# Kernel optimization log

Measured on AMD Instinct MI355X. Metric: run time of the kernel, lower is better.

The kernel has to match this reference:

```python
import jax, jax.numpy as jnp
import numpy as np

IMG = 32            # feature-map side == image_size
B, HC = 8, 3        # batch, hint channels
C, NH, L = 256, 8, 8  # model_channels, nhead, num_encoder_layers
DFF = 1025
HIN = IMG * 8       # hint resolution (three stride-2 convs => /8)
NEIGH = (7, 7)
CONV_SHAPES = [(16, HC), (16, 16), (32, 16), (32, 32), (96, 32), (96, 96), (256, 96), (C, 256)]
STRIDES = [1, 1, 2, 1, 2, 1, 2, 1]


def setup_inputs() -> dict:
    key = jax.random.key(0)
    ks = jax.random.split(key, 32)
    inp = {"hint": jax.random.normal(ks[0], (B, HC, HIN, HIN), jnp.float32)}
    for i, (co, ci) in enumerate(CONV_SHAPES):
        inp[f"conv_w{i}"] = jax.random.normal(ks[1 + i], (co, ci, 3, 3), jnp.float32) * 0.05
    base = 9
    def p(shape, j):
        return jax.random.normal(ks[base + j], (L,) + shape, jnp.float32) * 0.02
    inp["in_proj_w"] = p((3 * C, C), 0)
    inp["in_proj_b"] = p((3 * C,), 1)
    inp["out_w"] = p((C, C), 2)
    inp["out_b"] = p((C,), 3)
    inp["lin1_w"] = p((DFF, C), 4)
    inp["lin1_b"] = p((DFF,), 5)
    inp["lin2_w"] = p((C, DFF), 6)
    inp["lin2_b"] = p((C,), 7)
    inp["ln1_w"] = jnp.ones((L, C), jnp.float32)
    inp["ln1_b"] = jnp.zeros((L, C), jnp.float32)
    inp["ln2_w"] = jnp.ones((L, C), jnp.float32)
    inp["ln2_b"] = jnp.zeros((L, C), jnp.float32)
    return inp


def _conv(x, w, s):
    # torch Conv2d(k=3, padding=1, stride=s, bias=False)
    return jax.lax.conv_general_dilated(x, w, (s, s), [(1, 1), (1, 1)],
                                        dimension_numbers=("NCHW", "OIHW", "NCHW"))


def _sine_pos(h, w, c):
    # DETR/UniAD PositionEmbeddingSine (normalize=False, temperature=1e4) -> (h*w, c)
    npf = c // 2
    y = jnp.broadcast_to(jnp.arange(1, h + 1, dtype=jnp.float32)[:, None], (h, w))
    x = jnp.broadcast_to(jnp.arange(1, w + 1, dtype=jnp.float32)[None, :], (h, w))
    dim_t = 10000.0 ** (2.0 * (jnp.arange(npf, dtype=jnp.float32) // 2) / npf)
    px = x[..., None] / dim_t
    py = y[..., None] / dim_t
    px = jnp.stack([jnp.sin(px[..., 0::2]), jnp.cos(px[..., 1::2])], -1).reshape(h, w, npf)
    py = jnp.stack([jnp.sin(py[..., 0::2]), jnp.cos(py[..., 1::2])], -1).reshape(h, w, npf)
    return jnp.concatenate([py, px], -1).reshape(h * w, c)


def _neigh_mask(h, w, hm, wm):
    # vectorized version of generate_mask: 0 inside the hm x wm neighborhood, -inf outside
    ih = jnp.arange(h)
    iw = jnp.arange(w)
    dh = jnp.abs(ih[:, None] - ih[None, :]) <= hm // 2   # (h, h)
    dw = jnp.abs(iw[:, None] - iw[None, :]) <= wm // 2   # (w, w)
    allowed = (dh[:, None, :, None] & dw[None, :, None, :]).reshape(h * w, h * w)
    return jnp.where(allowed, 0.0, -1e9).astype(jnp.float32)


def _ln(x, g, b):
    mu = x.mean(-1, keepdims=True)
    v = ((x - mu) ** 2).mean(-1, keepdims=True)
    return (x - mu) / jnp.sqrt(v + 1e-5) * g + b


def _forward(hint, conv_ws, params):
    x = hint
    for i, (w, s) in enumerate(zip(conv_ws, STRIDES)):
        x = _conv(x, w, s)
        if i < len(conv_ws) - 1:
            x = jax.nn.silu(x)
    b, c, h, w = x.shape
    src = x.reshape(b, c, h * w).transpose(0, 2, 1)          # (B, N, C), N h-major
    pos = _sine_pos(h, w, c)[None]                           # (1, N, C)
    mask = _neigh_mask(h, w, *NEIGH)                         # (N, N)
    dh = c // NH
    scale = 1.0 / np.sqrt(dh).astype(np.float32)

    def layer(s, p):
        ipw, ipb, ow, ob, l1w, l1b, l2w, l2b, g1, b1, g2, b2 = p
        qk_in = s + pos
        q = (qk_in @ ipw[:c].T + ipb[:c]).reshape(b, -1, NH, dh)
        k = (qk_in @ ipw[c:2 * c].T + ipb[c:2 * c]).reshape(b, -1, NH, dh)
        v = (s @ ipw[2 * c:].T + ipb[2 * c:]).reshape(b, -1, NH, dh)
        sc = jnp.einsum('bnhd,bmhd->bhnm', q, k) * scale + mask
        a = jax.nn.softmax(sc, -1)
        ctx = jnp.einsum('bhnm,bmhd->bnhd', a, v).reshape(b, -1, c)
        s = _ln(s + ctx @ ow.T + ob, g1, b1)                 # post-norm
        ff = jax.nn.relu(s @ l1w.T + l1b) @ l2w.T + l2b      # dropout inactive (eval)
        return _ln(s + ff, g2, b2), None

    src, _ = jax.lax.scan(layer, src, params)
    return src.transpose(0, 2, 1).reshape(b, c, h, w)        # '(h w) b c -> b c h w'


def reference(hint, conv_w0, conv_w1, conv_w2, conv_w3, conv_w4, conv_w5, conv_w6, conv_w7,
              in_proj_w, in_proj_b, out_w, out_b, lin1_w, lin1_b, lin2_w, lin2_b,
              ln1_w, ln1_b, ln2_w, ln2_b):
    conv_ws = (conv_w0, conv_w1, conv_w2, conv_w3, conv_w4, conv_w5, conv_w6, conv_w7)
    params = (in_proj_w, in_proj_b, out_w, out_b, lin1_w, lin1_b, lin2_w, lin2_b,
              ln1_w, ln1_b, ln2_w, ln2_b)
    return _forward(hint, conv_ws, params)
```

## Files before the change

kernel.cpp:

```cpp
#include <hip/hip_runtime.h>
#include <hip/hip_bf16.h>


typedef __bf16 bf16x8 __attribute__((ext_vector_type(8)));
typedef float f32x4 __attribute__((ext_vector_type(4)));
typedef unsigned short us8v __attribute__((ext_vector_type(8)));

__device__ __forceinline__ unsigned short f2bf(float f) {
  unsigned int u = __float_as_uint(f);
  unsigned int r = (u + 0x7fffu + ((u >> 16) & 1u)) >> 16;
  return (unsigned short)r;
}
__device__ __forceinline__ float bf2f(unsigned short h) {
  return __uint_as_float(((unsigned int)h) << 16);
}

#define GLD16(src, dst)                                                        \
  __builtin_amdgcn_global_load_lds(                                            \
      (const __attribute__((address_space(1))) unsigned int*)(src),            \
      (__attribute__((address_space(3))) unsigned int*)(dst), 16, 0, 0)

template<int BM, int BN, int NT, int MODE, int LNF = 0, int KTC = 0>
__global__ __launch_bounds__(NT) void k_gemm(
    const unsigned short* __restrict__ A, int lda,
    const unsigned short* __restrict__ Bw, int ldb,
    const float* __restrict__ bias, const float* __restrict__ posadd,
    float* __restrict__ C, unsigned short* __restrict__ Cb, int ldc,
    int K, int Nstore, int act, int omode, long long zsB, long long zsC,
    const unsigned short* __restrict__ zpage, int Ci, int Hi, int stride, int lw,
    int divm, int divs, const float* __restrict__ lng, const float* __restrict__ lnb)
{
  constexpr int NW = NT / 64;
  constexpr int NWN = (NT == 512) ? 4 : ((BN >= 128) ? 2 : 1);
  constexpr int NWM = NW / NWN;
  constexpr int WM = BM / NWM, WN = BN / NWN;
  constexpr int MF = WM / 16, NF = WN / 16;
  constexpr int AIS = (BM * 8) / NT;
  constexpr int BIS = (BN * 8) / NT;
  __shared__ unsigned short lA[2][BM * 64];
  __shared__ unsigned short lB[2][BN * 64];
  int tid = threadIdx.x, lane = tid & 63, wid = tid >> 6;
  int bm = blockIdx.x * BM, bn = blockIdx.y * BN;
  const unsigned short* Bz = Bw + (size_t)blockIdx.z * zsB;

  int j = (lane & 7) ^ (lane >> 3);
  int e8 = (j & 3) << 3;
  int halfl = j >> 2;

  size_t arow[AIS], brow[BIS];
  int hb[AIS], wb[AIS];
  size_t ab[AIS];
#pragma unroll
  for (int i = 0; i < AIS; ++i) {
    int rr = (wid + i * NW) * 8 + (lane >> 3);
    if constexpr (MODE == 0) {
      arow[i] = (size_t)(bm + rr) * lda + (j << 3);
    } else {
      int pos = bm + rr;
      int b = pos >> (2 * lw);
      int rem = pos & ((1 << (2 * lw)) - 1);
      int ho = rem >> lw, wo = rem & ((1 << lw) - 1);
      hb[i] = ho * stride - 1;
      wb[i] = wo * stride - 1;
      ab[i] = (size_t)b * Hi * Hi * Ci;
    }
  }
#pragma unroll
  for (int i = 0; i < BIS; ++i)
    brow[i] = (size_t)(bn + (wid + i * NW) * 8 + (lane >> 3)) * ldb + (j << 3);

  auto stage = [&](int buf, int kt) {
    if constexpr (MODE == 1) {
      int s0 = kt * 2, s1 = s0 + 1;
      int t0 = (s0 * divm) >> divs, t1 = (s1 * divm) >> divs;
      int cipw = Ci >> 5;
      int cc0 = (s0 - t0 * cipw) << 5, cc1 = (s1 - t1 * cipw) << 5;
      int kh0 = (t0 * 171) >> 9, kw0 = t0 - kh0 * 3;
      int kh1 = (t1 * 171) >> 9, kw1 = t1 - kh1 * 3;
      int kh = halfl ? kh1 : kh0;
      int kw = halfl ? kw1 : kw0;
      int cco = halfl ? cc1 : cc0;
      bool tv = (halfl ? t1 : t0) < 9;
#pragma unroll
      for (int i = 0; i < AIS; ++i) {
        int hi = hb[i] + kh, wi = wb[i] + kw;
        const unsigned short* ap =
            (tv && (unsigned)hi < (unsigned)Hi && (unsigned)wi < (unsigned)Hi)
                ? (A + ab[i] + (size_t)(hi * Hi + wi) * Ci + cco + e8)
                : zpage;
        GLD16(ap, &lA[buf][(wid + i * NW) * 512]);
      }
    } else {
#pragma unroll
      for (int i = 0; i < AIS; ++i)
        GLD16(A + arow[i] + kt * 64, &lA[buf][(wid + i * NW) * 512]);
    }
#pragma unroll
    for (int i = 0; i < BIS; ++i)
      GLD16(Bz + brow[i] + kt * 64, &lB[buf][(wid + i * NW) * 512]);
  };

  f32x4 acc[MF][NF];
#pragma unroll
  for (int m = 0; m < MF; ++m)
#pragma unroll
    for (int n = 0; n < NF; ++n)
#pragma unroll
      for (int q = 0; q < 4; ++q) acc[m][n][q] = 0.f;

  int wn = wid % NWN, wm = wid / NWN;
  int r0 = wm * WM + (lane & 15);
  int c0 = wn * WN + (lane & 15);
  int sl0 = (((lane >> 4)) ^ (lane & 7)) << 3;
  int sl1 = (((lane >> 4) + 4) ^ (lane & 7)) << 3;
  const int nkt = (KTC > 0) ? KTC : (K >> 6);
  int cur = 0;
  stage(0, 0);
#pragma unroll
  for (int kt = 0; kt < nkt; ++kt) {
    if (kt + 1 < nkt) {
      stage(cur ^ 1, kt + 1);
      asm volatile("s_waitcnt vmcnt(%0)" : : "n"(AIS + BIS) : "memory");
    } else {
      asm volatile("s_waitcnt vmcnt(0)" : : : "memory");
    }
    __builtin_amdgcn_s_barrier();
    asm volatile("" ::: "memory");
    bf16x8 a0[MF], a1[MF], b0[NF], b1[NF];
#pragma unroll
    for (int m = 0; m < MF; ++m) {
      a0[m] = *(const bf16x8*)&lA[cur][(r0 + m * 16) * 64 + sl0];
      a1[m] = *(const bf16x8*)&lA[cur][(r0 + m * 16) * 64 + sl1];
    }
#pragma unroll
    for (int n = 0; n < NF; ++n) {
      b0[n] = *(const bf16x8*)&lB[cur][(c0 + n * 16) * 64 + sl0];
      b1[n] = *(const bf16x8*)&lB[cur][(c0 + n * 16) * 64 + sl1];
    }
#pragma unroll
    for (int m = 0; m < MF; ++m)
#pragma unroll
      for (int n = 0; n < NF; ++n)
        acc[m][n] = __builtin_amdgcn_mfma_f32_16x16x32_bf16(a0[m], b0[n], acc[m][n], 0, 0, 0);
#pragma unroll
    for (int m = 0; m < MF; ++m)
#pragma unroll
      for (int n = 0; n < NF; ++n)
        acc[m][n] = __builtin_amdgcn_mfma_f32_16x16x32_bf16(a1[m], b1[n], acc[m][n], 0, 0, 0);
    asm volatile("" ::: "memory");
    __builtin_amdgcn_s_barrier();
    cur ^= 1;
  }

  int colb = bn + wn * WN + (lane & 15);
  int rowb = bm + wm * WM + ((lane >> 4) << 2);
  float* Cz = C ? C + (size_t)blockIdx.z * zsC : nullptr;
  unsigned short* Cbz = Cb ? Cb + (size_t)blockIdx.z * zsC : nullptr;
#pragma unroll
  for (int n = 0; n < NF; ++n) {
    int col = colb + n * 16;
    if (col >= Nstore) continue;
    float bs = bias ? bias[col] : 0.f;
#pragma unroll
    for (int m = 0; m < MF; ++m) {
#pragma unroll
      for (int q = 0; q < 4; ++q) {
        int row = rowb + m * 16 + q;
        float v = acc[m][n][q] + bs;
        if (posadd && col < 512) v += posadd[((row & 1023) << 9) + col];
        if (act == 1) v = fmaxf(v, 0.f);
        else if (act == 2) v = v / (1.f + __expf(-v));
        size_t off = (size_t)row * ldc + col;
        if (omode == 0) Cz[off] = v;
        else if (omode == 1) Cbz[off] = f2bf(v);
        else { Cz[off] = v; Cbz[off] = f2bf(v); }
      }
    }
  }
}

__global__ __launch_bounds__(256) void k_mlp(
    const unsigned short* __restrict__ ctx, const unsigned short* __restrict__ wo,
    const float* __restrict__ ob,
    const unsigned short* __restrict__ w1, const float* __restrict__ b1,
    const unsigned short* __restrict__ w2, const float* __restrict__ b2,
    float* __restrict__ src, unsigned short* __restrict__ sbo,
    const float* __restrict__ g1, const float* __restrict__ lb1,
    const float* __restrict__ g2, const float* __restrict__ lb2)
{
  __shared__ unsigned short aT[4][32 * 64];
  __shared__ unsigned short lB[4][128 * 64];
  __shared__ unsigned short ffl[32][1160];
  __shared__ float red[2][32][2];
  int tid = threadIdx.x, lane = tid & 63, wid = tid >> 6;
  int bm = blockIdx.x << 5;
  int rsrc = lane >> 3;
  int jj8 = ((lane & 7) ^ rsrc) << 3;

  {
    int rr = wid * 8 + rsrc;
    const unsigned short* ap = ctx + (size_t)(bm + rr) * 256 + jj8;
#pragma unroll
    for (int kt = 0; kt < 4; ++kt)
      GLD16(ap + kt * 64, &aT[kt][wid * 512]);
  }

  auto issue = [&](int s) {
    const unsigned short* base;
    int ld, coloff, row0;
    if (s < 8)       { base = wo; ld = 256;  coloff = (s >> 1) * 64; row0 = (s & 1) * 128; }
    else if (s < 44) { int t = s - 8;  base = w1; ld = 256;  coloff = (t & 3) * 64; row0 = (t >> 2) * 128; }
    else             { int t = s - 44; base = w2; ld = 1152; coloff = (t >> 1) * 64; row0 = (t & 1) * 128; }
    int buf = s & 3;
#pragma unroll
    for (int i = 0; i < 4; ++i) {
      int rr = row0 + (wid + i * 4) * 8 + rsrc;
      GLD16(base + (size_t)rr * ld + coloff + jj8, &lB[buf][(wid + i * 4) * 512]);
    }
  };
  issue(0); issue(1); issue(2); issue(3);

  int wn = wid & 1, wm = wid >> 1;
  int r0 = wm * 16 + (lane & 15);
  int sl0 = ((lane >> 4) ^ (lane & 7)) << 3;
  int sl1 = (((lane >> 4) + 4) ^ (lane & 7)) << 3;
  int kqa = (lane >> 4) << 3;
  int cbase = wn * 16 + (lane & 15);
  int rowl = wm * 16 + ((lane >> 4) << 2);

  f32x4 acco[8];
#pragma unroll
  for (int m = 0; m < 8; ++m)
#pragma unroll
    for (int q = 0; q < 4; ++q) acco[m][q] = 0.f;
#pragma unroll
  for (int s = 0; s < 8; ++s) {
    const int kt = s >> 1, rh = s & 1;
    asm volatile("s_waitcnt vmcnt(12)" ::: "memory");
    __builtin_amdgcn_s_barrier();
    asm volatile("" ::: "memory");
    bf16x8 a0 = *(const bf16x8*)&aT[kt][r0 * 64 + sl0];
    bf16x8 a1 = *(const bf16x8*)&aT[kt][r0 * 64 + sl1];
    bf16x8 b0v[4], b1v[4];
#pragma unroll
    for (int nn = 0; nn < 4; ++nn) {
      int rowb = cbase + nn * 32;
      b0v[nn] = *(const bf16x8*)&lB[s & 3][rowb * 64 + sl0];
      b1v[nn] = *(const bf16x8*)&lB[s & 3][rowb * 64 + sl1];
    }
    __builtin_amdgcn_s_setprio(1);
#pragma unroll
    for (int nn = 0; nn < 4; ++nn)
      acco[rh * 4 + nn] = __builtin_amdgcn_mfma_f32_16x16x32_bf16(a0, b0v[nn], acco[rh * 4 + nn], 0, 0, 0);
#pragma unroll
    for (int nn = 0; nn < 4; ++nn)
      acco[rh * 4 + nn] = __builtin_amdgcn_mfma_f32_16x16x32_bf16(a1, b1v[nn], acco[rh * 4 + nn], 0, 0, 0);
    __builtin_amdgcn_s_setprio(0);
    asm volatile("" ::: "memory");
    __builtin_amdgcn_s_barrier();
    issue(s + 4);
  }

  float resid[8][4];
  {
    float x[8][4];
    float sums[4] = {0.f, 0.f, 0.f, 0.f}, sqs[4] = {0.f, 0.f, 0.f, 0.f};
#pragma unroll
    for (int m = 0; m < 8; ++m) {
      int col = ((m >> 2) << 7) + cbase + ((m & 3) << 5);
      float bs = ob[col];
#pragma unroll
      for (int q = 0; q < 4; ++q) {
        float v = acco[m][q] + bs + src[(size_t)(bm + rowl + q) * 256 + col];
        x[m][q] = v;
        sums[q] += v;
        sqs[q] += v * v;
      }
    }
#pragma unroll
    for (int q = 0; q < 4; ++q) {
      sums[q] += __shfl_xor(sums[q], 1); sqs[q] += __shfl_xor(sqs[q], 1);
      sums[q] += __shfl_xor(sums[q], 2); sqs[q] += __shfl_xor(sqs[q], 2);
      sums[q] += __shfl_xor(sums[q], 4); sqs[q] += __shfl_xor(sqs[q], 4);
      sums[q] += __shfl_xor(sums[q], 8); sqs[q] += __shfl_xor(sqs[q], 8);
    }
    if ((lane & 15) == 0) {
#pragma unroll
      for (int q = 0; q < 4; ++q) {
        red[wn][rowl + q][0] = sums[q];
        red[wn][rowl + q][1] = sqs[q];
      }
    }
    asm volatile("s_waitcnt lgkmcnt(0)" ::: "memory");
    __builtin_amdgcn_s_barrier();
    asm volatile("" ::: "memory");
#pragma unroll
    for (int q = 0; q < 4; ++q) {
      float ts = sums[q] + red[wn ^ 1][rowl + q][0];
      float tq = sqs[q] + red[wn ^ 1][rowl + q][1];
      float mu = ts * (1.f / 256.f);
      float var = tq * (1.f / 256.f) - mu * mu;
      float rs = rsqrtf(var + 1e-5f);
      int r = rowl + q;
#pragma unroll
      for (int m = 0; m < 8; ++m) {
        int col = ((m >> 2) << 7) + cbase + ((m & 3) << 5);
        float o = (x[m][q] - mu) * rs * g1[col] + lb1[col];
        resid[m][q] = o;
        int kt = col >> 6, jjc = (col >> 3) & 7, e = col & 7;
        aT[kt][r * 64 + ((jjc ^ (r & 7)) << 3) + e] = f2bf(o);
      }
    }
  }
  asm volatile("s_waitcnt lgkmcnt(0)" ::: "memory");
  __builtin_amdgcn_s_barrier();
  asm volatile("" ::: "memory");

  for (int ny = 0; ny < 9; ++ny) {
    f32x4 acc1[4];
#pragma unroll
    for (int nn = 0; nn < 4; ++nn)
#pragma unroll
      for (int q = 0; q < 4; ++q) acc1[nn][q] = 0.f;
#pragma unroll
    for (int kt = 0; kt < 4; ++kt) {
      int s = 8 + ny * 4 + kt;
      asm volatile("s_waitcnt vmcnt(12)" ::: "memory");
      __builtin_amdgcn_s_barrier();
      asm volatile("" ::: "memory");
      bf16x8 a0 = *(const bf16x8*)&aT[kt][r0 * 64 + sl0];
      bf16x8 a1 = *(const bf16x8*)&aT[kt][r0 * 64 + sl1];
      bf16x8 b0v[4], b1v[4];
#pragma unroll
      for (int nn = 0; nn < 4; ++nn) {
        int rowb = cbase + nn * 32;
        b0v[nn] = *(const bf16x8*)&lB[s & 3][rowb * 64 + sl0];
        b1v[nn] = *(const bf16x8*)&lB[s & 3][rowb * 64 + sl1];
      }
      __builtin_amdgcn_s_setprio(1);
#pragma unroll
      for (int nn = 0; nn < 4; ++nn)
        acc1[nn] = __builtin_amdgcn_mfma_f32_16x16x32_bf16(a0, b0v[nn], acc1[nn], 0, 0, 0);
#pragma unroll
      for (int nn = 0; nn < 4; ++nn)
        acc1[nn] = __builtin_amdgcn_mfma_f32_16x16x32_bf16(a1, b1v[nn], acc1[nn], 0, 0, 0);
      __builtin_amdgcn_s_setprio(0);
      asm volatile("" ::: "memory");
      __builtin_amdgcn_s_barrier();
      issue(s + 4);
    }
#pragma unroll
    for (int nn = 0; nn < 4; ++nn) {
      int col = ny * 128 + cbase + nn * 32;
      float bs = b1[col];
#pragma unroll
      for (int q = 0; q < 4; ++q)
        ffl[rowl + q][col] = f2bf(fmaxf(acc1[nn][q] + bs, 0.f));
    }
  }
  asm volatile("s_waitcnt lgkmcnt(0)" ::: "memory");

  f32x4 acc[8];
#pragma unroll
  for (int m = 0; m < 8; ++m)
#pragma unroll
    for (int q = 0; q < 4; ++q) acc[m][q] = 0.f;
  for (int kt = 0; kt < 18; ++kt) {
#pragma unroll
    for (int rh = 0; rh < 2; ++rh) {
      int t = kt * 2 + rh;
      if (t <= 32) { asm volatile("s_waitcnt vmcnt(12)" ::: "memory"); }
      else if (t == 33) { asm volatile("s_waitcnt vmcnt(8)" ::: "memory"); }
      else if (t == 34) { asm volatile("s_waitcnt vmcnt(4)" ::: "memory"); }
      else { asm volatile("s_waitcnt vmcnt(0)" ::: "memory"); }
      __builtin_amdgcn_s_barrier();
      asm volatile("" ::: "memory");
      bf16x8 a0 = *(const bf16x8*)&ffl[r0][kt * 64 + kqa];
      bf16x8 a1 = *(const bf16x8*)&ffl[r0][kt * 64 + 32 + kqa];
      bf16x8 b0v[4], b1v[4];
#pragma unroll
      for (int nn = 0; nn < 4; ++nn) {
        int rowb = cbase + nn * 32;
        b0v[nn] = *(const bf16x8*)&lB[(44 + t) & 3][rowb * 64 + sl0];
        b1v[nn] = *(const bf16x8*)&lB[(44 + t) & 3][rowb * 64 + sl1];
      }
      __builtin_amdgcn_s_setprio(1);
#pragma unroll
      for (int nn = 0; nn < 4; ++nn)
        acc[rh * 4 + nn] = __builtin_amdgcn_mfma_f32_16x16x32_bf16(a0, b0v[nn], acc[rh * 4 + nn], 0, 0, 0);
#pragma unroll
      for (int nn = 0; nn < 4; ++nn)
        acc[rh * 4 + nn] = __builtin_amdgcn_mfma_f32_16x16x32_bf16(a1, b1v[nn], acc[rh * 4 + nn], 0, 0, 0);
      __builtin_amdgcn_s_setprio(0);
      asm volatile("" ::: "memory");
      __builtin_amdgcn_s_barrier();
      if (t < 32) issue(48 + t);
    }
  }

  float x[8][4];
  float sums[4] = {0.f, 0.f, 0.f, 0.f}, sqs[4] = {0.f, 0.f, 0.f, 0.f};
#pragma unroll
  for (int m = 0; m < 8; ++m) {
    int col = ((m >> 2) << 7) + cbase + ((m & 3) << 5);
    float bs = b2[col];
#pragma unroll
    for (int q = 0; q < 4; ++q) {
      float v = acc[m][q] + bs + resid[m][q];
      x[m][q] = v;
      sums[q] += v;
      sqs[q] += v * v;
    }
  }
#pragma unroll
  for (int q = 0; q < 4; ++q) {
    sums[q] += __shfl_xor(sums[q], 1); sqs[q] += __shfl_xor(sqs[q], 1);
    sums[q] += __shfl_xor(sums[q], 2); sqs[q] += __shfl_xor(sqs[q], 2);
    sums[q] += __shfl_xor(sums[q], 4); sqs[q] += __shfl_xor(sqs[q], 4);
    sums[q] += __shfl_xor(sums[q], 8); sqs[q] += __shfl_xor(sqs[q], 8);
  }
  __syncthreads();
  if ((lane & 15) == 0) {
#pragma unroll
    for (int q = 0; q < 4; ++q) {
      red[wn][rowl + q][0] = sums[q];
      red[wn][rowl + q][1] = sqs[q];
    }
  }
  __syncthreads();
#pragma unroll
  for (int q = 0; q < 4; ++q) {
    float ts = sums[q] + red[wn ^ 1][rowl + q][0];
    float tq = sqs[q] + red[wn ^ 1][rowl + q][1];
    float mu = ts * (1.f / 256.f);
    float var = tq * (1.f / 256.f) - mu * mu;
    float rs = rsqrtf(var + 1e-5f);
    int row = bm + rowl + q;
#pragma unroll
    for (int m = 0; m < 8; ++m) {
      int col = ((m >> 2) << 7) + cbase + ((m & 3) << 5);
      float o = (x[m][q] - mu) * rs * g2[col] + lb2[col];
      src[(size_t)row * 256 + col] = o;
      sbo[(size_t)row * 256 + col] = f2bf(o);
    }
  }
}

__global__ __launch_bounds__(256) void k_conv0(
    const float* __restrict__ x, const float* __restrict__ w,
    unsigned short* __restrict__ y)
{
  __shared__ float ws[16][28];
  int tid = threadIdx.x;
  for (int u = tid; u < 432; u += 256) {
    int co = u / 27, k = u - co * 27;
    int t = k / 3, ci = k - t * 3;
    ws[co][k] = w[((size_t)co * 3 + ci) * 9 + t];
  }
  __syncthreads();
  int h = blockIdx.x, b = blockIdx.y, wo = tid;
  float xin[3][3][3];
#pragma unroll
  for (int ci = 0; ci < 3; ++ci)
#pragma unroll
    for (int kh = 0; kh < 3; ++kh) {
      int hi = h + kh - 1;
#pragma unroll
      for (int kw = 0; kw < 3; ++kw) {
        int wi = wo + kw - 1;
        xin[ci][kh][kw] = ((unsigned)hi < 256u && (unsigned)wi < 256u)
            ? x[(((size_t)b * 3 + ci) << 16) + (hi << 8) + wi] : 0.f;
      }
    }
  float acc[16] = {};
#pragma unroll
  for (int t = 0; t < 9; ++t) {
    const int kh = t / 3, kw = t % 3;
#pragma unroll
    for (int ci = 0; ci < 3; ++ci) {
      float xv = xin[ci][kh][kw];
#pragma unroll
      for (int co = 0; co < 16; ++co)
        acc[co] = fmaf(xv, ws[co][t * 3 + ci], acc[co]);
    }
  }
  us8v o0, o1, zv;
#pragma unroll
  for (int q = 0; q < 8; ++q) {
    float v0 = acc[q];     v0 = v0 / (1.f + __expf(-v0)); o0[q] = f2bf(v0);
    float v1 = acc[q + 8]; v1 = v1 / (1.f + __expf(-v1)); o1[q] = f2bf(v1);
    zv[q] = 0;
  }
  unsigned short* yp = y + ((((size_t)b << 16) + (h << 8) + wo) << 5);
  *(us8v*)(yp) = o0; *(us8v*)(yp + 8) = o1;
  *(us8v*)(yp + 16) = zv; *(us8v*)(yp + 24) = zv;
}

template<int S>
__global__ __launch_bounds__(256) void k_conv_direct(
    const unsigned short* __restrict__ x, const unsigned short* __restrict__ wp,
    int ldw, unsigned short* __restrict__ y, int Hi, int Ho, int Wo, int lwt)
{
  constexpr int HR = 7 * S + 3;
  constexpr int HC = 15 * S + 3;
  constexpr int HP = HR * HC;
  __shared__ unsigned short xs[HP * 40];
  __shared__ unsigned short wsh[32 * 312];
  int tid = threadIdx.x, lane = tid & 63, wv = tid >> 6;
  int b = blockIdx.y;
  int tr = blockIdx.x >> lwt, tc = blockIdx.x & ((1 << lwt) - 1);
  int hi0 = tr * 8 * S - 1, wi0 = tc * 16 * S - 1;

  for (int u = tid; u < HP * 8; u += 256) {
    int pix = u >> 3, part = u & 7;
    int hr = pix / HC, hcc = pix - hr * HC;
    int hi = hi0 + hr, wi = wi0 + hcc;
    ushort4 v = {0, 0, 0, 0};
    if ((unsigned)hi < (unsigned)Hi && (unsigned)wi < (unsigned)Hi)
      v = *(const ushort4*)(x + ((size_t)(b * Hi + hi) * Hi + wi) * 32 + part * 4);
    *(ushort4*)(&xs[pix * 40 + part * 4]) = v;
  }
  for (int u = tid; u < 2304; u += 256) {
    int co = u / 72, kk = (u - co * 72) * 4;
    *(ushort4*)(&wsh[co * 312 + kk]) = *(const ushort4*)(wp + (size_t)co * ldw + kk);
  }
  __syncthreads();

  int cL = lane & 15, kq = (lane >> 4) << 3;
  f32x4 acc[2][2];
#pragma unroll
  for (int m = 0; m < 2; ++m)
#pragma unroll
    for (int n = 0; n < 2; ++n)
#pragma unroll
      for (int q = 0; q < 4; ++q) acc[m][n][q] = 0.f;

#pragma unroll
  for (int tap = 0; tap < 9; ++tap) {
    const int kh = tap / 3, kw = tap % 3;
    bf16x8 af[2], bfr[2];
#pragma unroll
    for (int m = 0; m < 2; ++m) {
      int hr = (wv * 2 + m) * S + kh;
      int hc = cL * S + kw;
      af[m] = *(const bf16x8*)&xs[(hr * HC + hc) * 40 + kq];
    }
#pragma unroll
    for (int n = 0; n < 2; ++n)
      bfr[n] = *(const bf16x8*)&wsh[(cL + n * 16) * 312 + tap * 32 + kq];
#pragma unroll
    for (int m = 0; m < 2; ++m)
#pragma unroll
      for (int n = 0; n < 2; ++n)
        acc[m][n] = __builtin_amdgcn_mfma_f32_16x16x32_bf16(af[m], bfr[n], acc[m][n], 0, 0, 0);
  }

  int wo0 = tc * 16 + ((lane >> 4) << 2);
#pragma unroll
  for (int m = 0; m < 2; ++m) {
    int ho = tr * 8 + wv * 2 + m;
#pragma unroll
    for (int n = 0; n < 2; ++n) {
      int co = cL + n * 16;
#pragma unroll
      for (int q = 0; q < 4; ++q) {
        float v = acc[m][n][q];
        v = v / (1.f + __expf(-v));
        y[((size_t)(b * Ho + ho) * Wo + wo0 + q) * 32 + co] = f2bf(v);
      }
    }
  }
}

struct WP8 { const float* w[8]; unsigned short* q[8]; };
__global__ __launch_bounds__(256) void k_wperm_all(WP8 p)
{
  const int CoPs[8]  = {128, 32, 32, 32, 128, 128, 256, 256};
  const int CiRs[8]  = {3, 16, 16, 32, 32, 96, 96, 256};
  const int CiPs[8]  = {3, 32, 32, 32, 32, 96, 96, 256};
  const int Kpads[8] = {64, 288, 288, 288, 320, 896, 896, 2304};
  const int Cos[8]   = {16, 16, 32, 32, 96, 96, 256, 256};
  int i = blockIdx.y + 1;
  const float* w = p.w[i];
  unsigned short* wp = p.q[i];
  int Kpad = Kpads[i], CiP = CiPs[i], CiR = CiRs[i], Co = Cos[i];
  int total = CoPs[i] * Kpad;
  for (int idx = blockIdx.x * 256 + threadIdx.x; idx < total; idx += gridDim.x * 256) {
    int co = idx / Kpad, k = idx - co * Kpad;
    int t = k / CiP, ci = k - t * CiP;
    float v = 0.f;
    if (co < Co && t < 9 && ci < CiR) v = w[((size_t)co * CiR + ci) * 9 + t];
    wp[idx] = f2bf(v);
  }
}

struct PrepArgs {
  const float *ipw, *outw, *l1w, *l2w, *l1b;
  unsigned short *wqkvb, *outwb, *l1wb, *l2wb, *posb;
  float *l1bp;
};
__global__ __launch_bounds__(256) void k_prep(PrepArgs a)
{
  int seg = blockIdx.y;
  int idx0 = blockIdx.x * 256 + threadIdx.x;
  int stride = gridDim.x * 256;
  if (seg == 0) {
    for (int i = idx0; i < 8 * 768 * 256; i += stride) a.wqkvb[i] = f2bf(a.ipw[i]);
  } else if (seg == 1) {
    for (int i = idx0; i < 8 * 256 * 256; i += stride) a.outwb[i] = f2bf(a.outw[i]);
  } else if (seg == 2) {
    for (int i = idx0; i < 8 * 1152 * 256; i += stride) {
      int l = i / (1152 * 256), r = (i >> 8) % 1152, c = i & 255;
      float v = (r < 1025) ? a.l1w[((size_t)l * 1025 + r) * 256 + c] : 0.f;
      a.l1wb[i] = f2bf(v);
    }
  } else if (seg == 3) {
    for (int i = idx0; i < 8 * 256 * 1152; i += stride) {
      int l = i / (256 * 1152), rc = i % (256 * 1152), r = rc / 1152, c = rc - (rc / 1152) * 1152;
      float v = (c < 1025) ? a.l2w[((size_t)l * 256 + r) * 1025 + c] : 0.f;
      a.l2wb[i] = f2bf(v);
    }
  } else if (seg == 4) {
    for (int i = idx0; i < 8 * 1152; i += stride) {
      int l = i / 1152, c = i - l * 1152;
      a.l1bp[i] = (c < 1025) ? a.l1b[l * 1025 + c] : 0.f;
    }
  } else {
    for (int i = idx0; i < 1024 * 256; i += stride) {
      int n = i >> 8, c = i & 255;
      int ih = n >> 5, iw = n & 31;
      float coord = (c < 128) ? (float)(ih + 1) : (float)(iw + 1);
      int cc = c & 127;
      float e = (float)((cc >> 1) << 1) * (1.f / 128.f);
      float t = coord / powf(10000.f, e);
      a.posb[i] = f2bf((cc & 1) ? cosf(t) : sinf(t));
    }
  }
}

__global__ __launch_bounds__(256) void k_attn(
    const unsigned short* __restrict__ qkv, unsigned short* __restrict__ ctx,
    const unsigned short* __restrict__ wwo, const unsigned short* __restrict__ ww1,
    const unsigned short* __restrict__ ww2)
{
  __shared__ unsigned short k_ldsu[848 * 8];
  __shared__ unsigned short v_lds[848 * 8];
  __shared__ float p_lds[64 * 50];
  int bx = blockIdx.x;
  int b = bx >> 4, tile = bx & 15;
  int th8 = ((tile >> 2) << 3), tw8 = ((tile & 3) << 3);
  int g = blockIdx.y;
  int tid = threadIdx.x, lane = tid & 63, wid = tid >> 6;
  int h0e = max(th8 - 3, 0), h1e = min(th8 + 10, 31);
  int w0e = max(tw8 - 3, 0), w1e = min(tw8 + 10, 31);
  int nh = h1e - h0e + 1, nw = w1e - w0e + 1;
  int nkeys = nh * nw, nslots = nkeys * 4;
  unsigned int magic = (65536u + (unsigned)nw - 1u) / (unsigned)nw;
  size_t qbase = (size_t)((unsigned)b << 10) * 768;

#pragma unroll
  for (int i = 0; i < 4; ++i) {
    int base = i * 256 + wid * 64;
    if (base < 784) {
      int s = min(base + lane, nslots - 1);
      int uidx = s >> 2, chunk = s & 3;
      int hh = (int)(((unsigned)uidx * magic) >> 16);
      int ww = uidx - hh * nw;
      hh += h0e; ww += w0e;
      const unsigned short* rp = qkv + qbase + (size_t)((hh << 5) + ww) * 768 + (g << 5) + chunk * 8;
      GLD16(rp + 256, &k_ldsu[base * 8]);
      GLD16(rp + 512, &v_lds[base * 8]);
    }
  }

  us8v wt[3];
  bool wvld[3] = {false, false, false};
  {
    int bid = bx + (g << 7);
    int slice = bid >> 3;
    const size_t TOT = 65536 + 294912 + 294912;
#pragma unroll
    for (int p = 0; p < 3; ++p) {
      size_t off = (size_t)slice * 5120 + (size_t)p * 2048 + (size_t)tid * 8;
      if (off < TOT) {
        const unsigned short* wp;
        if (off < 65536) wp = wwo + off;
        else if (off < 65536 + 294912) wp = ww1 + (off - 65536);
        else wp = ww2 + (off - 65536 - 294912);
        wt[p] = *(const us8v*)wp;
        wvld[p] = true;
      }
    }
  }
  __syncthreads();

  int q = tid >> 2, dq = tid & 3;
  int qh = th8 + (q >> 3), qw = tw8 + (q & 7);
  const float scale = 0.17677669529663687f;
  const unsigned short* qp = qkv + qbase + (size_t)((qh << 5) + qw) * 768 + (g << 5) + dq * 8;
  us8v uq = *(const us8v*)qp;
  float qr[8];
#pragma unroll
  for (int t = 0; t < 8; ++t) qr[t] = bf2f(uq[t]) * scale;

  int rbase[7], cofs[7];
  bool rval[7], cval[7];
#pragma unroll
  for (int d = 0; d < 7; ++d) {
    int mh = qh - 3 + d;
    rval[d] = (unsigned)mh < 32u;
    rbase[d] = (mh - h0e) * nw;
    int mw = qw - 3 + d;
    cval[d] = (unsigned)mw < 32u;
    cofs[d] = mw - w0e;
  }

  float m = -1e30f;
#pragma unroll
  for (int kk = 0; kk < 49; ++kk) {
    const int d7 = kk / 7, r7 = kk % 7;
    bool valid = rval[d7] && cval[r7];
    int uidx = valid ? (rbase[d7] + cofs[r7]) : 0;
    us8v uk = *(const us8v*)&k_ldsu[uidx * 32 + dq * 8];
    float d = 0.f;
#pragma unroll
    for (int t = 0; t < 8; ++t) d = fmaf(qr[t], bf2f(uk[t]), d);
    d += __shfl_xor(d, 1);
    d += __shfl_xor(d, 2);
    float s_kk = valid ? d : -1e30f;
    m = fmaxf(m, s_kk);
    if (dq == (kk & 3)) p_lds[q * 50 + kk] = s_kk;
  }
  float sum = 0.f;
  for (int kk = dq; kk < 49; kk += 4) {
    float e = __expf(p_lds[q * 50 + kk] - m);
    p_lds[q * 50 + kk] = e;
    sum += e;
  }
  sum += __shfl_xor(sum, 1);
  sum += __shfl_xor(sum, 2);
  float inv = 1.f / sum;

  float acc[8] = {};
#pragma unroll
  for (int kk = 0; kk < 49; ++kk) {
    const int d7 = kk / 7, r7 = kk % 7;
    int uidx = (rval[d7] && cval[r7]) ? (rbase[d7] + cofs[r7]) : 0;
    float pb = p_lds[q * 50 + kk];
    us8v uv = *(const us8v*)&v_lds[uidx * 32 + dq * 8];
#pragma unroll
    for (int t = 0; t < 8; ++t) acc[t] = fmaf(pb, bf2f(uv[t]), acc[t]);
  }
  unsigned short* op = ctx + ((size_t)((b << 10) + (qh << 5) + qw) << 8) + (g << 5) + dq * 8;
  us8v out;
#pragma unroll
  for (int t = 0; t < 8; ++t) out[t] = f2bf(acc[t] * inv);
  *(us8v*)op = out;

#pragma unroll
  for (int p = 0; p < 3; ++p)
    if (wvld[p]) asm volatile("" :: "v"(wt[p]));
}

__global__ void k_nxc_to_cxn(const float* __restrict__ x, float* __restrict__ y)
{
  __shared__ float t[32][33];
  int b = blockIdx.z;
  int c0 = blockIdx.x * 32, n0 = blockIdx.y * 32;
  int tx = threadIdx.x, ty = threadIdx.y;
  t[ty][tx] = x[((size_t)(b * 1024 + n0 + ty)) * 256 + c0 + tx];
  __syncthreads();
  y[((size_t)(b * 256 + c0 + ty)) * 1024 + n0 + tx] = t[tx][ty];
}

extern "C" void kernel_launch(void* const* d_in, const int* in_sizes, int n_in,
                              void* d_out, int out_size, void* d_ws, size_t ws_size,
                              hipStream_t stream)
{
  const float* hint = (const float*)d_in[0];
  const float* cw[8];
  for (int i = 0; i < 8; ++i) cw[i] = (const float*)d_in[1 + i];
  const float* ipw  = (const float*)d_in[9];
  const float* ipb  = (const float*)d_in[10];
  const float* outw = (const float*)d_in[11];
  const float* outb = (const float*)d_in[12];
  const float* l1w  = (const float*)d_in[13];
  const float* l1b  = (const float*)d_in[14];
  const float* l2w  = (const float*)d_in[15];
  const float* l2b  = (const float*)d_in[16];
  const float* g1   = (const float*)d_in[17];
  const float* b1   = (const float*)d_in[18];
  const float* g2   = (const float*)d_in[19];
  const float* b2   = (const float*)d_in[20];

  float* ws = (float*)d_ws;
  size_t off = 0;
  float* bufA = ws + off; off += 8388608;
  float* bufB = ws + off; off += 8388608;
  float* src  = ws + off; off += 2097152;
  unsigned short* srcb = (unsigned short*)(ws + off); off += 1048576;
  unsigned short* posb = (unsigned short*)(ws + off); off += 131072;
  float* posqk = ws + off; off += 4194304;
  unsigned short* wqkvb = (unsigned short*)(ws + off); off += 786432;
  unsigned short* outwb = (unsigned short*)(ws + off); off += 262144;
  unsigned short* l1wb  = (unsigned short*)(ws + off); off += 1179648;
  unsigned short* l2wb  = (unsigned short*)(ws + off); off += 1179648;
  float* l1bp = ws + off; off += 9216;
  unsigned short* cwp[8];
  const int CoPs[8]  = {128, 32, 32, 32, 128, 128, 256, 256};
  const int Kpads[8] = {64, 288, 288, 288, 320, 896, 896, 2304};
  for (int i = 0; i < 8; ++i) { cwp[i] = (unsigned short*)(ws + off); off += ((size_t)CoPs[i] * Kpads[i] + 1) / 2; }
  unsigned short* zpage = (unsigned short*)(ws + off); off += 64;

  hipMemsetAsync(zpage, 0, 256, stream);

  PrepArgs pa;
  pa.ipw = ipw; pa.outw = outw; pa.l1w = l1w; pa.l2w = l2w; pa.l1b = l1b;
  pa.wqkvb = wqkvb; pa.outwb = outwb; pa.l1wb = l1wb; pa.l2wb = l2wb;
  pa.posb = posb; pa.l1bp = l1bp;
  k_prep<<<dim3(256, 6), 256, 0, stream>>>(pa);
  WP8 wpargs;
  for (int i = 0; i < 8; ++i) { wpargs.w[i] = cw[i]; wpargs.q[i] = cwp[i]; }
  k_wperm_all<<<dim3(64, 7), 256, 0, stream>>>(wpargs);

  unsigned short* bufAu = (unsigned short*)bufA;
  unsigned short* bufBu = (unsigned short*)bufB;

#define GEMM_TAIL nullptr, 0, 0, 0, 0, 0, 0, nullptr, nullptr
  k_conv0<<<dim3(256, 8), 256, 0, stream>>>(hint, cw[0], bufAu);
  k_conv_direct<1><<<dim3(512, 8), 256, 0, stream>>>(bufAu, cwp[1], 288, bufBu, 256, 256, 256, 4);
  k_conv_direct<2><<<dim3(128, 8), 256, 0, stream>>>(bufBu, cwp[2], 288, bufAu, 256, 128, 128, 3);
  k_conv_direct<1><<<dim3(128, 8), 256, 0, stream>>>(bufAu, cwp[3], 288, bufBu, 128, 128, 128, 3);
  k_gemm<128, 128, 512, 1, 0, 5><<<dim3(256, 1), 512, 0, stream>>>(
      bufBu, 0, cwp[4], 320, nullptr, nullptr, nullptr, bufAu, 96, 320, 96, 2, 1,
      0, 0, zpage, 32, 128, 2, 6, 1, 0, nullptr, nullptr);
  k_gemm<128, 128, 512, 1, 0, 14><<<dim3(256, 1), 512, 0, stream>>>(
      bufAu, 0, cwp[5], 896, nullptr, nullptr, nullptr, bufBu, 96, 896, 96, 2, 1,
      0, 0, zpage, 96, 64, 1, 6, 171, 9, nullptr, nullptr);
  k_gemm<64, 128, 512, 1, 0, 14><<<dim3(128, 2), 512, 0, stream>>>(
      bufBu, 0, cwp[6], 896, nullptr, nullptr, nullptr, bufAu, 256, 896, 256, 2, 1,
      0, 0, zpage, 96, 64, 2, 5, 171, 9, nullptr, nullptr);
  k_gemm<64, 128, 512, 1><<<dim3(128, 2), 512, 0, stream>>>(
      bufAu, 0, cwp[7], 2304, nullptr, nullptr, src, srcb, 256, 2304, 256, 0, 2,
      0, 0, zpage, 256, 32, 1, 5, 1, 3, nullptr, nullptr);

  k_gemm<64, 128, 512, 0, 0, 4><<<dim3(16, 4, 8), 512, 0, stream>>>(
      posb, 256, wqkvb, 256, nullptr, nullptr, posqk, nullptr, 512, 256, 512, 0, 0,
      196608LL, 524288LL, GEMM_TAIL);

  unsigned short* qkvb = bufAu;
  unsigned short* ctx  = (unsigned short*)(bufA + 3145728);

  for (int l = 0; l < 8; ++l) {
    const unsigned short* wqkv_l = wqkvb + (size_t)l * 768 * 256;
    const float* ipb_l  = ipb  + (size_t)l * 768;
    const unsigned short* outw_l = outwb + (size_t)l * 256 * 256;
    const float* outb_l = outb + (size_t)l * 256;
    const unsigned short* l1w_l = l1wb + (size_t)l * 1152 * 256;
    const float* l1b_l  = l1bp + (size_t)l * 1152;
    const unsigned short* l2w_l = l2wb + (size_t)l * 256 * 1152;
    const float* l2b_l  = l2b  + (size_t)l * 256;
    const float* posqk_l = posqk + (size_t)l * 524288;
    const float* g1_l = g1 + l * 256; const float* b1_l = b1 + l * 256;
    const float* g2_l = g2 + l * 256; const float* b2_l = b2 + l * 256;

    k_gemm<64, 128, 512, 0, 0, 4><<<dim3(128, 6), 512, 0, stream>>>(
        srcb, 256, wqkv_l, 256, ipb_l, posqk_l, nullptr, qkvb, 768, 256, 768, 0, 1,
        0, 0, GEMM_TAIL);
    k_attn<<<dim3(128, 8), 256, 0, stream>>>(qkvb, ctx, outw_l, l1w_l, l2w_l);
    k_mlp<<<dim3(256), 256, 0, stream>>>(
        ctx, outw_l, outb_l, l1w_l, l1b_l, l2w_l, l2b_l,
        src, srcb, g1_l, b1_l, g2_l, b2_l);
  }

  k_nxc_to_cxn<<<dim3(8, 32, 8), dim3(32, 32), 0, stream>>>(src, (float*)d_out);
}
```

Before: 840.0 us.

## Halve k_mlp row tile to 16 and double grid with 2-stage weight pipeline

The fused out-proj/FFN/LayerNorm kernel now processes 16 rows per block instead of 32, so it launches 512 blocks. That is meant to fill more CUs on the GPU, since 256 blocks leaves many of them idle. Each wave now owns a 32-column slice rather than a 2x2 split, and LayerNorm partial sums are reduced across 4 waves. The weight staging buffer drops from 4 stages to 2 to cut LDS use, which reduces prefetch depth. Each weight tile is also now reused across half as many rows, doubling total weight traffic from L2.

```diff
diff --git a/kernel.cpp b/kernel.cpp
--- a/kernel.cpp
+++ b/kernel.cpp
@@ -188,21 +188,24 @@
     const float* __restrict__ g1, const float* __restrict__ lb1,
     const float* __restrict__ g2, const float* __restrict__ lb2)
 {
-  __shared__ unsigned short aT[4][32 * 64];
-  __shared__ unsigned short lB[4][128 * 64];
-  __shared__ unsigned short ffl[32][1160];
-  __shared__ float red[2][32][2];
+  __shared__ unsigned short aT[4][16 * 64];
+  __shared__ unsigned short lB[2][128 * 64];
+  __shared__ unsigned short ffl[16][1160];
+  __shared__ float red[4][16][2];
   int tid = threadIdx.x, lane = tid & 63, wid = tid >> 6;
-  int bm = blockIdx.x << 5;
+  int bm = blockIdx.x << 4;
   int rsrc = lane >> 3;
   int jj8 = ((lane & 7) ^ rsrc) << 3;
 
   {
-    int rr = wid * 8 + rsrc;
-    const unsigned short* ap = ctx + (size_t)(bm + rr) * 256 + jj8;
-#pragma unroll
-    for (int kt = 0; kt < 4; ++kt)
-      GLD16(ap + kt * 64, &aT[kt][wid * 512]);
+#pragma unroll
+    for (int i = 0; i < 2; ++i) {
+      int c = i * 64 + lane;
+      int row = c >> 3, slot = c & 7;
+      int sch = slot ^ (row & 7);
+      GLD16(ctx + (size_t)(bm + row) * 256 + wid * 64 + (sch << 3),
+            &aT[wid][i * 512]);
+    }
   }
 
   auto issue = [&](int s) {
@@ -211,63 +214,69 @@
     if (s < 8)       { base = wo; ld = 256;  coloff = (s >> 1) * 64; row0 = (s & 1) * 128; }
     else if (s < 44) { int t = s - 8;  base = w1; ld = 256;  coloff = (t & 3) * 64; row0 = (t >> 2) * 128; }
     else             { int t = s - 44; base = w2; ld = 1152; coloff = (t >> 1) * 64; row0 = (t & 1) * 128; }
-    int buf = s & 3;
+    int buf = s & 1;
 #pragma unroll
     for (int i = 0; i < 4; ++i) {
       int rr = row0 + (wid + i * 4) * 8 + rsrc;
       GLD16(base + (size_t)rr * ld + coloff + jj8, &lB[buf][(wid + i * 4) * 512]);
     }
   };
-  issue(0); issue(1); issue(2); issue(3);
-
-  int wn = wid & 1, wm = wid >> 1;
-  int r0 = wm * 16 + (lane & 15);
+  issue(0); issue(1);
+
+  int r0 = lane & 15;
   int sl0 = ((lane >> 4) ^ (lane & 7)) << 3;
   int sl1 = (((lane >> 4) + 4) ^ (lane & 7)) << 3;
   int kqa = (lane >> 4) << 3;
-  int cbase = wn * 16 + (lane & 15);
-  int rowl = wm * 16 + ((lane >> 4) << 2);
-
-  f32x4 acco[8];
-#pragma unroll
-  for (int m = 0; m < 8; ++m)
+  int rowl = (lane >> 4) << 2;
+
+  auto stage_top = [&](int s) {
+    if (s == 79) { asm volatile("s_waitcnt vmcnt(0)" ::: "memory"); }
+    else         { asm volatile("s_waitcnt vmcnt(4)" ::: "memory"); }
+    __builtin_amdgcn_s_barrier();
+    asm volatile("" ::: "memory");
+  };
+  auto stage_bot = [&](int s) {
+    asm volatile("" ::: "memory");
+    __builtin_amdgcn_s_barrier();
+    if (s + 2 < 80) issue(s + 2);
+  };
+
+  f32x4 acco[4];
+#pragma unroll
+  for (int m = 0; m < 4; ++m)
 #pragma unroll
     for (int q = 0; q < 4; ++q) acco[m][q] = 0.f;
 #pragma unroll
   for (int s = 0; s < 8; ++s) {
     const int kt = s >> 1, rh = s & 1;
-    asm volatile("s_waitcnt vmcnt(12)" ::: "memory");
-    __builtin_amdgcn_s_barrier();
-    asm volatile("" ::: "memory");
+    stage_top(s);
     bf16x8 a0 = *(const bf16x8*)&aT[kt][r0 * 64 + sl0];
     bf16x8 a1 = *(const bf16x8*)&aT[kt][r0 * 64 + sl1];
-    bf16x8 b0v[4], b1v[4];
-#pragma unroll
-    for (int nn = 0; nn < 4; ++nn) {
-      int rowb = cbase + nn * 32;
-      b0v[nn] = *(const bf16x8*)&lB[s & 3][rowb * 64 + sl0];
-      b1v[nn] = *(const bf16x8*)&lB[s & 3][rowb * 64 + sl1];
+    bf16x8 b0v[2], b1v[2];
+#pragma unroll
+    for (int nn = 0; nn < 2; ++nn) {
+      int rowb = wid * 32 + nn * 16 + (lane & 15);
+      b0v[nn] = *(const bf16x8*)&lB[s & 1][rowb * 64 + sl0];
+      b1v[nn] = *(const bf16x8*)&lB[s & 1][rowb * 64 + sl1];
     }
     __builtin_amdgcn_s_setprio(1);
 #pragma unroll
-    for (int nn = 0; nn < 4; ++nn)
-      acco[rh * 4 + nn] = __builtin_amdgcn_mfma_f32_16x16x32_bf16(a0, b0v[nn], acco[rh * 4 + nn], 0, 0, 0);
-#pragma unroll
-    for (int nn = 0; nn < 4; ++nn)
-      acco[rh * 4 + nn] = __builtin_amdgcn_mfma_f32_16x16x32_bf16(a1, b1v[nn], acco[rh * 4 + nn], 0, 0, 0);
+    for (int nn = 0; nn < 2; ++nn)
+      acco[rh * 2 + nn] = __builtin_amdgcn_mfma_f32_16x16x32_bf16(a0, b0v[nn], acco[rh * 2 + nn], 0, 0, 0);
+#pragma unroll
+    for (int nn = 0; nn < 2; ++nn)
+      acco[rh * 2 + nn] = __builtin_amdgcn_mfma_f32_16x16x32_bf16(a1, b1v[nn], acco[rh * 2 + nn], 0, 0, 0);
     __builtin_amdgcn_s_setprio(0);
-    asm volatile("" ::: "memory");
-    __builtin_amdgcn_s_barrier();
-    issue(s + 4);
-  }
-
-  float resid[8][4];
+    stage_bot(s);
+  }
+
+  float resid[4][4];
   {
-    float x[8][4];
+    float x[4][4];
     float sums[4] = {0.f, 0.f, 0.f, 0.f}, sqs[4] = {0.f, 0.f, 0.f, 0.f};
 #pragma unroll
-    for (int m = 0; m < 8; ++m) {
-      int col = ((m >> 2) << 7) + cbase + ((m & 3) << 5);
+    for (int m = 0; m < 4; ++m) {
+      int col = (m >> 1) * 128 + wid * 32 + (m & 1) * 16 + (lane & 15);
       float bs = ob[col];
 #pragma unroll
       for (int q = 0; q < 4; ++q) {
@@ -287,8 +296,8 @@
     if ((lane & 15) == 0) {
 #pragma unroll
       for (int q = 0; q < 4; ++q) {
-        red[wn][rowl + q][0] = sums[q];
-        red[wn][rowl + q][1] = sqs[q];
+        red[wid][rowl + q][0] = sums[q];
+        red[wid][rowl + q][1] = sqs[q];
       }
     }
     asm volatile("s_waitcnt lgkmcnt(0)" ::: "memory");
@@ -296,15 +305,15 @@
     asm volatile("" ::: "memory");
 #pragma unroll
     for (int q = 0; q < 4; ++q) {
-      float ts = sums[q] + red[wn ^ 1][rowl + q][0];
-      float tq = sqs[q] + red[wn ^ 1][rowl + q][1];
+      int r = rowl + q;
+      float ts = red[0][r][0] + red[1][r][0] + red[2][r][0] + red[3][r][0];
+      float tq = red[0][r][1] + red[1][r][1] + red[2][r][1] + red[3][r][1];
       float mu = ts * (1.f / 256.f);
       float var = tq * (1.f / 256.f) - mu * mu;
       float rs = rsqrtf(var + 1e-5f);
-      int r = rowl + q;
-#pragma unroll
-      for (int m = 0; m < 8; ++m) {
-        int col = ((m >> 2) << 7) + cbase + ((m & 3) << 5);
+#pragma unroll
+      for (int m = 0; m < 4; ++m) {
+        int col = (m >> 1) * 128 + wid * 32 + (m & 1) * 16 + (lane & 15);
         float o = (x[m][q] - mu) * rs * g1[col] + lb1[col];
         resid[m][q] = o;
         int kt = col >> 6, jjc = (col >> 3) & 7, e = col & 7;
@@ -317,41 +326,37 @@
   asm volatile("" ::: "memory");
 
   for (int ny = 0; ny < 9; ++ny) {
-    f32x4 acc1[4];
-#pragma unroll
-    for (int nn = 0; nn < 4; ++nn)
+    f32x4 acc1[2];
+#pragma unroll
+    for (int nn = 0; nn < 2; ++nn)
 #pragma unroll
       for (int q = 0; q < 4; ++q) acc1[nn][q] = 0.f;
 #pragma unroll
     for (int kt = 0; kt < 4; ++kt) {
       int s = 8 + ny * 4 + kt;
-      asm volatile("s_waitcnt vmcnt(12)" ::: "memory");
-      __builtin_amdgcn_s_barrier();
-      asm volatile("" ::: "memory");
+      stage_top(s);
       bf16x8 a0 = *(const bf16x8*)&aT[kt][r0 * 64 + sl0];
       bf16x8 a1 = *(const bf16x8*)&aT[kt][r0 * 64 + sl1];
-      bf16x8 b0v[4], b1v[4];
-#pragma unroll
-      for (int nn = 0; nn < 4; ++nn) {
-        int rowb = cbase + nn * 32;
-        b0v[nn] = *(const bf16x8*)&lB[s & 3][rowb * 64 + sl0];
-        b1v[nn] = *(const bf16x8*)&lB[s & 3][rowb * 64 + sl1];
+      bf16x8 b0v[2], b1v[2];
+#pragma unroll
+      for (int nn = 0; nn < 2; ++nn) {
+        int rowb = wid * 32 + nn * 16 + (lane & 15);
+        b0v[nn] = *(const bf16x8*)&lB[s & 1][rowb * 64 + sl0];
+        b1v[nn] = *(const bf16x8*)&lB[s & 1][rowb * 64 + sl1];
       }
       __builtin_amdgcn_s_setprio(1);
 #pragma unroll
-      for (int nn = 0; nn < 4; ++nn)
+      for (int nn = 0; nn < 2; ++nn)
         acc1[nn] = __builtin_amdgcn_mfma_f32_16x16x32_bf16(a0, b0v[nn], acc1[nn], 0, 0, 0);
 #pragma unroll
-      for (int nn = 0; nn < 4; ++nn)
+      for (int nn = 0; nn < 2; ++nn)
         acc1[nn] = __builtin_amdgcn_mfma_f32_16x16x32_bf16(a1, b1v[nn], acc1[nn], 0, 0, 0);
       __builtin_amdgcn_s_setprio(0);
-      asm volatile("" ::: "memory");
-      __builtin_amdgcn_s_barrier();
-      issue(s + 4);
-    }
-#pragma unroll
-    for (int nn = 0; nn < 4; ++nn) {
-      int col = ny * 128 + cbase + nn * 32;
+      stage_bot(s);
+    }
+#pragma unroll
+    for (int nn = 0; nn < 2; ++nn) {
+      int col = ny * 128 + wid * 32 + nn * 16 + (lane & 15);
       float bs = b1[col];
 #pragma unroll
       for (int q = 0; q < 4; ++q)
@@ -360,53 +365,46 @@
   }
   asm volatile("s_waitcnt lgkmcnt(0)" ::: "memory");
 
-  f32x4 acc[8];
-#pragma unroll
-  for (int m = 0; m < 8; ++m)
-#pragma unroll
-    for (int q = 0; q < 4; ++q) acc[m][q] = 0.f;
+  f32x4 acc2[4];
+#pragma unroll
+  for (int m = 0; m < 4; ++m)
+#pragma unroll
+    for (int q = 0; q < 4; ++q) acc2[m][q] = 0.f;
   for (int kt = 0; kt < 18; ++kt) {
 #pragma unroll
     for (int rh = 0; rh < 2; ++rh) {
-      int t = kt * 2 + rh;
-      if (t <= 32) { asm volatile("s_waitcnt vmcnt(12)" ::: "memory"); }
-      else if (t == 33) { asm volatile("s_waitcnt vmcnt(8)" ::: "memory"); }
-      else if (t == 34) { asm volatile("s_waitcnt vmcnt(4)" ::: "memory"); }
-      else { asm volatile("s_waitcnt vmcnt(0)" ::: "memory"); }
-      __builtin_amdgcn_s_barrier();
-      asm volatile("" ::: "memory");
+      int s = 44 + kt * 2 + rh;
+      stage_top(s);
       bf16x8 a0 = *(const bf16x8*)&ffl[r0][kt * 64 + kqa];
       bf16x8 a1 = *(const bf16x8*)&ffl[r0][kt * 64 + 32 + kqa];
-      bf16x8 b0v[4], b1v[4];
-#pragma unroll
-      for (int nn = 0; nn < 4; ++nn) {
-        int rowb = cbase + nn * 32;
-        b0v[nn] = *(const bf16x8*)&lB[(44 + t) & 3][rowb * 64 + sl0];
-        b1v[nn] = *(const bf16x8*)&lB[(44 + t) & 3][rowb * 64 + sl1];
+      bf16x8 b0v[2], b1v[2];
+#pragma unroll
+      for (int nn = 0; nn < 2; ++nn) {
+        int rowb = wid * 32 + nn * 16 + (lane & 15);
+        b0v[nn] = *(const bf16x8*)&lB[s & 1][rowb * 64 + sl0];
+        b1v[nn] = *(const bf16x8*)&lB[s & 1][rowb * 64 + sl1];
       }
       __builtin_amdgcn_s_setprio(1);
 #pragma unroll
-      for (int nn = 0; nn < 4; ++nn)
-        acc[rh * 4 + nn] = __builtin_amdgcn_mfma_f32_16x16x32_bf16(a0, b0v[nn], acc[rh * 4 + nn], 0, 0, 0);
-#pragma unroll
-      for (int nn = 0; nn < 4; ++nn)
-        acc[rh * 4 + nn] = __builtin_amdgcn_mfma_f32_16x16x32_bf16(a1, b1v[nn], acc[rh * 4 + nn], 0, 0, 0);
+      for (int nn = 0; nn < 2; ++nn)
+        acc2[rh * 2 + nn] = __builtin_amdgcn_mfma_f32_16x16x32_bf16(a0, b0v[nn], acc2[rh * 2 + nn], 0, 0, 0);
+#pragma unroll
+      for (int nn = 0; nn < 2; ++nn)
+        acc2[rh * 2 + nn] = __builtin_amdgcn_mfma_f32_16x16x32_bf16(a1, b1v[nn], acc2[rh * 2 + nn], 0, 0, 0);
       __builtin_amdgcn_s_setprio(0);
-      asm volatile("" ::: "memory");
-      __builtin_amdgcn_s_barrier();
-      if (t < 32) issue(48 + t);
-    }
-  }
-
-  float x[8][4];
+      stage_bot(s);
+    }
+  }
+
+  float x[4][4];
   float sums[4] = {0.f, 0.f, 0.f, 0.f}, sqs[4] = {0.f, 0.f, 0.f, 0.f};
 #pragma unroll
-  for (int m = 0; m < 8; ++m) {
-    int col = ((m >> 2) << 7) + cbase + ((m & 3) << 5);
+  for (int m = 0; m < 4; ++m) {
+    int col = (m >> 1) * 128 + wid * 32 + (m & 1) * 16 + (lane & 15);
     float bs = b2[col];
 #pragma unroll
     for (int q = 0; q < 4; ++q) {
-      float v = acc[m][q] + bs + resid[m][q];
+      float v = acc2[m][q] + bs + resid[m][q];
       x[m][q] = v;
       sums[q] += v;
       sqs[q] += v * v;
@@ -423,22 +421,23 @@
   if ((lane & 15) == 0) {
 #pragma unroll
     for (int q = 0; q < 4; ++q) {
-      red[wn][rowl + q][0] = sums[q];
-      red[wn][rowl + q][1] = sqs[q];
+      red[wid][rowl + q][0] = sums[q];
+      red[wid][rowl + q][1] = sqs[q];
     }
   }
   __syncthreads();
 #pragma unroll
   for (int q = 0; q < 4; ++q) {
-    float ts = sums[q] + red[wn ^ 1][rowl + q][0];
-    float tq = sqs[q] + red[wn ^ 1][rowl + q][1];
+    int r = rowl + q;
+    float ts = red[0][r][0] + red[1][r][0] + red[2][r][0] + red[3][r][0];
+    float tq = red[0][r][1] + red[1][r][1] + red[2][r][1] + red[3][r][1];
     float mu = ts * (1.f / 256.f);
     float var = tq * (1.f / 256.f) - mu * mu;
     float rs = rsqrtf(var + 1e-5f);
-    int row = bm + rowl + q;
-#pragma unroll
-    for (int m = 0; m < 8; ++m) {
-      int col = ((m >> 2) << 7) + cbase + ((m & 3) << 5);
+    int row = bm + r;
+#pragma unroll
+    for (int m = 0; m < 4; ++m) {
+      int col = (m >> 1) * 128 + wid * 32 + (m & 1) * 16 + (lane & 15);
       float o = (x[m][q] - mu) * rs * g2[col] + lb2[col];
       src[(size_t)row * 256 + col] = o;
       sbo[(size_t)row * 256 + col] = f2bf(o);
@@ -868,7 +867,7 @@
         srcb, 256, wqkv_l, 256, ipb_l, posqk_l, nullptr, qkvb, 768, 256, 768, 0, 1,
         0, 0, GEMM_TAIL);
     k_attn<<<dim3(128, 8), 256, 0, stream>>>(qkvb, ctx, outw_l, l1w_l, l2w_l);
-    k_mlp<<<dim3(256), 256, 0, stream>>>(
+    k_mlp<<<dim3(512), 256, 0, stream>>>(
         ctx, outw_l, outb_l, l1w_l, l1b_l, l2w_l, l2b_l,
         src, srcb, g1_l, b1_l, g2_l, b2_l);
   }
```

Measured after the change: 851.3 us. Within noise of the previous version (+1.3%).
